# Kernel tuning notes

Hardware: AMD Instinct MI355X
Metric: run time of the kernel (lower is better)

The kernel has to match this reference:

```python
import jax, jax.numpy as jnp
import numpy as np

OPS = jnp.array([[1,1,1],[1,1,-1],[1,-1,1],[1,-1,-1],[-1,1,1],[-1,1,-1],[-1,-1,1],[-1,-1,-1]], dtype=jnp.float32)  # [8,3] sign flips per eigenvector column

B, N, FN, FE, E = 1, 512, 8, 1, 32
D0 = 6 + FN  # layer-0 node embedding dim: framed (x,v) = 6 dims + node features


def setup_inputs() -> dict:
    key = jax.random.key(0)
    ks = jax.random.split(key, 24)
    rn = lambda k, shp, s=0.1: jax.random.normal(k, shp, jnp.float32) * s
    inp = {
        'node_feat': jax.random.normal(ks[0], (B, N, FN), jnp.float32),
        'edge_feat': jax.random.normal(ks[1], (B, N, N, FE), jnp.float32),
        'x': jax.random.normal(ks[2], (B, N, 3), jnp.float32),
        'v': jax.random.normal(ks[3], (B, N, 3), jnp.float32),
        # GNN layer 0 (input node dim D0)
        'e0_w1': rn(ks[4], (FE + 2 * D0, E)), 'e0_b1': jnp.zeros((E,), jnp.float32),
        'e0_w2': rn(ks[5], (E, E)), 'e0_b2': jnp.zeros((E,), jnp.float32),
        'n0_w1': rn(ks[6], (D0 + E, E)), 'n0_b1': jnp.zeros((E,), jnp.float32),
        'n0_w2': rn(ks[7], (E, E)), 'n0_b2': jnp.zeros((E,), jnp.float32),
        # GNN layer 1 (input node dim E)
        'e1_w1': rn(ks[8], (FE + 2 * E, E)), 'e1_b1': jnp.zeros((E,), jnp.float32),
        'e1_w2': rn(ks[9], (E, E)), 'e1_b2': jnp.zeros((E,), jnp.float32),
        'n1_w1': rn(ks[10], (E + E, E)), 'n1_b1': jnp.zeros((E,), jnp.float32),
        'n1_w2': rn(ks[11], (E, E)), 'n1_b2': jnp.zeros((E,), jnp.float32),
        # decoder: relu -> Linear(E,E) -> relu -> Linear(E,6)
        'dec_w1': rn(ks[12], (E, E)), 'dec_b1': jnp.zeros((E,), jnp.float32),
        'dec_w2': rn(ks[13], (E, 6)), 'dec_b2': jnp.zeros((6,), jnp.float32),
        # v_coef: relu -> Linear(E,E) -> relu -> Linear(E,1)
        'vc_w1': rn(ks[14], (E, E)), 'vc_b1': jnp.zeros((E,), jnp.float32),
        'vc_w2': rn(ks[15], (E, 1)), 'vc_b2': jnp.zeros((1,), jnp.float32),
    }
    return inp


def _gnn_layer(h, edge_feat, ew1, eb1, ew2, eb2, nw1, nb1, nw2, nb2):
    # h: [B,N,d]; edge_feat: [B,N,N,Fe]
    # Torch builds concat([edge_feat, h_j, h_i]) per (i,j) pair; we split W1 rows
    # to avoid materializing the [B,N,N,Fe+2d] concat (same math).
    Fe = edge_feat.shape[-1]
    d = h.shape[-1]
    pre_e = edge_feat @ ew1[:Fe]          # [B,N,N,E]
    pre_j = h @ ew1[Fe:Fe + d]            # [B,N,E], indexed by j
    pre_i = h @ ew1[Fe + d:]              # [B,N,E], indexed by i
    m = jax.nn.relu(pre_e + pre_j[:, None, :, :] + pre_i[:, :, None, :] + eb1)
    m = jax.nn.relu(m @ ew2 + eb2)        # [B,N,N,E]
    agg = m.sum(axis=2)                   # sum over neighbors j -> [B,N,E]
    dn = jax.nn.relu(h @ nw1[:d] + agg @ nw1[d:] + nb1)
    return dn @ nw2 + nb2                 # [B,N,E]


def reference(node_feat, edge_feat, x, v,
              e0_w1, e0_b1, e0_w2, e0_b2, n0_w1, n0_b1, n0_w2, n0_b2,
              e1_w1, e1_b1, e1_w2, e1_b2, n1_w1, n1_b1, n1_w2, n1_b2,
              dec_w1, dec_b1, dec_w2, dec_b2, vc_w1, vc_b1, vc_w2, vc_b2):
    # ---- create_frame (PCA frame averaging) ----
    center = x.mean(axis=1, keepdims=True)                 # [B,1,3]
    xc = x - center
    R = jnp.einsum('bni,bnj->bij', xc, xc)                 # [B,3,3]
    _, Vv = jnp.linalg.eigh(R)                             # eigenvectors, ascending (like torch.symeig)
    F_ops = jax.lax.stop_gradient(OPS[None, :, None, :] * Vv[:, None, :, :])  # [B,8,3,3]
    center = jax.lax.stop_gradient(center)
    xc = x - center
    fx = jnp.einsum('boji,bnj->obni', F_ops, xc)           # [8,B,N,3] (F_ops^T applied)
    fv = jnp.einsum('boji,bnj->obni', F_ops, v)            # [8,B,N,3]
    nf = jnp.broadcast_to(node_feat[None], (8,) + node_feat.shape)
    h0 = jnp.concatenate([fx, fv, nf], axis=-1)            # [8,B,N,6+FN]

    l0 = (e0_w1, e0_b1, e0_w2, e0_b2, n0_w1, n0_b1, n0_w2, n0_b2)
    l1 = (e1_w1, e1_b1, e1_w2, e1_b2, n1_w1, n1_b1, n1_w2, n1_b2)
    frames = []
    for i in range(8):  # small fixed frame count; loop keeps N^2 intermediates per-frame
        hi = _gnn_layer(h0[i], edge_feat, *l0)
        hi = _gnn_layer(hi, edge_feat, *l1)
        frames.append(hi)
    h_out = jnp.stack(frames)                              # [8,B,N,E]

    # ---- decoder + invert_frame ----
    s = jax.nn.relu(jax.nn.relu(h_out) @ dec_w1 + dec_b1)
    spatial_out = s @ dec_w2 + dec_b2                      # [8,B,N,6]
    so = jnp.transpose(spatial_out, (1, 0, 2, 3))          # [B,8,N,6]
    dx = jnp.einsum('boij,bonj->bni', F_ops, so[..., :3]) / 8.0
    dv = jnp.einsum('boij,bonj->bni', F_ops, so[..., 3:]) / 8.0

    h_mean = h_out.mean(axis=0)                            # [B,N,E]
    coef = jax.nn.relu(jax.nn.relu(h_mean) @ vc_w1 + vc_b1) @ vc_w2 + vc_b2  # [B,N,1]
    v_out = v + dv
    x_out = x + v_out * coef + dx
    return (h_mean, edge_feat, x_out, v_out)
```

## Files before the change

### kernel.cpp

```cpp
#include <hip/hip_runtime.h>
#include <hip/hip_bf16.h>
#include <hip/hip_fp16.h>
#include <math.h>

#define NN 512

typedef _Float16 f16x8 __attribute__((ext_vector_type(8)));
typedef float    f32x4 __attribute__((ext_vector_type(4)));

__global__ void __launch_bounds__(256) frame_kernel(
    const float* __restrict__ x, float* __restrict__ FR,
    const float* __restrict__ e0w1, const float* __restrict__ e1w1,
    const float* __restrict__ e0w2, const float* __restrict__ e1w2,
    _Float16* __restrict__ WEH0, _Float16* __restrict__ WEH1,
    _Float16* __restrict__ W2F0, _Float16* __restrict__ W2F1) {
    __shared__ double red[4][9];
    int t = threadIdx.x;
    double s[9] = {0,0,0,0,0,0,0,0,0};
    for (int n = t; n < NN; n += 256) {
        double X = x[n*3+0], Y = x[n*3+1], Z = x[n*3+2];
        s[0]+=X; s[1]+=Y; s[2]+=Z;
        s[3]+=X*X; s[4]+=X*Y; s[5]+=X*Z; s[6]+=Y*Y; s[7]+=Y*Z; s[8]+=Z*Z;
    }
    #pragma unroll
    for (int m = 1; m < 64; m <<= 1) {
        #pragma unroll
        for (int q = 0; q < 9; ++q) s[q] += __shfl_xor(s[q], m);
    }
    int wave = t >> 6, lane = t & 63;
    if (lane == 0) {
        #pragma unroll
        for (int q = 0; q < 9; ++q) red[wave][q] = s[q];
    }
    __syncthreads();
    if (wave == 1) {
        int l15 = lane & 15, kb = (lane >> 4) * 8;
        #pragma unroll
        for (int e = 0; e < 8; ++e) {
            W2F0[lane*16 + e]     = (_Float16)e0w2[(kb+e)*32 + l15];
            W2F0[lane*16 + 8 + e] = (_Float16)e0w2[(kb+e)*32 + l15 + 16];
            W2F1[lane*16 + e]     = (_Float16)e1w2[(kb+e)*32 + l15];
            W2F1[lane*16 + 8 + e] = (_Float16)e1w2[(kb+e)*32 + l15 + 16];
        }
        if (lane < 32) { WEH0[lane] = (_Float16)e0w1[lane]; WEH1[lane] = (_Float16)e1w1[lane]; }
    }
    if (t == 0) {
        double S[9];
        #pragma unroll
        for (int q = 0; q < 9; ++q) S[q] = red[0][q]+red[1][q]+red[2][q]+red[3][q];
        double cx = S[0]/512.0, cy = S[1]/512.0, cz = S[2]/512.0;
        double A[3][3];
        A[0][0]=S[3]-512.0*cx*cx; A[0][1]=S[4]-512.0*cx*cy; A[0][2]=S[5]-512.0*cx*cz;
        A[1][1]=S[6]-512.0*cy*cy; A[1][2]=S[7]-512.0*cy*cz; A[2][2]=S[8]-512.0*cz*cz;
        A[1][0]=A[0][1]; A[2][0]=A[0][2]; A[2][1]=A[1][2];
        double V[3][3] = {{1,0,0},{0,1,0},{0,0,1}};
        for (int sweep = 0; sweep < 8; ++sweep) {
            double off = fabs(A[0][1]) + fabs(A[0][2]) + fabs(A[1][2]);
            double dia = fabs(A[0][0]) + fabs(A[1][1]) + fabs(A[2][2]);
            if (off < 1e-14 * (dia + 1e-300)) break;
            for (int p = 0; p < 3; ++p) for (int q = p+1; q < 3; ++q) {
                double apq = A[p][q];
                if (fabs(apq) < 1e-300) continue;
                double tau = (A[q][q] - A[p][p]) / (2.0 * apq);
                double tt = (tau >= 0 ? 1.0 : -1.0) / (fabs(tau) + sqrt(1.0 + tau*tau));
                double cc = 1.0 / sqrt(1.0 + tt*tt), ss = tt * cc;
                double apq2 = apq;
                A[p][p] = A[p][p] - tt * apq2;
                A[q][q] = A[q][q] + tt * apq2;
                A[p][q] = 0.0; A[q][p] = 0.0;
                for (int k = 0; k < 3; ++k) if (k != p && k != q) {
                    double akp = A[k][p], akq = A[k][q];
                    A[k][p] = cc*akp - ss*akq; A[p][k] = A[k][p];
                    A[k][q] = ss*akp + cc*akq; A[q][k] = A[k][q];
                }
                for (int k = 0; k < 3; ++k) {
                    double vkp = V[k][p], vkq = V[k][q];
                    V[k][p] = cc*vkp - ss*vkq;
                    V[k][q] = ss*vkp + cc*vkq;
                }
            }
        }
        double ev[3] = {A[0][0], A[1][1], A[2][2]};
        int idx[3] = {0,1,2};
        for (int a = 0; a < 2; ++a) for (int b = a+1; b < 3; ++b)
            if (ev[idx[b]] < ev[idx[a]]) { int tmp = idx[a]; idx[a] = idx[b]; idx[b] = tmp; }
        FR[0] = (float)cx; FR[1] = (float)cy; FR[2] = (float)cz;
        for (int r = 0; r < 3; ++r)
            for (int c = 0; c < 3; ++c)
                FR[3 + r*3 + c] = (float)V[r][idx[c]];
    }
}

__global__ void __launch_bounds__(256) pre0_kernel(const float* __restrict__ x,
                                                   const float* __restrict__ v,
                                                   const float* __restrict__ nf,
                                                   const float* __restrict__ FR,
                                                   const float* __restrict__ ew1,
                                                   const float* __restrict__ eb1,
                                                   float* __restrict__ H0,
                                                   _Float16* __restrict__ PJ,
                                                   _Float16* __restrict__ PIB) {
    int t = blockIdx.x * 256 + threadIdx.x;
    int c = t & 31, row = t >> 5;
    int o = row >> 9, j = row & 511;
    float hrow[14];
    float xc0 = x[j*3+0] - FR[0], xc1 = x[j*3+1] - FR[1], xc2 = x[j*3+2] - FR[2];
    float v0 = v[j*3+0], v1 = v[j*3+1], v2 = v[j*3+2];
    #pragma unroll
    for (int i = 0; i < 3; ++i) {
        float sgn = ((o >> (2 - i)) & 1) ? -1.f : 1.f;
        float px = FR[3 + 0*3 + i]*xc0 + FR[3 + 1*3 + i]*xc1 + FR[3 + 2*3 + i]*xc2;
        float pv = FR[3 + 0*3 + i]*v0  + FR[3 + 1*3 + i]*v1  + FR[3 + 2*3 + i]*v2;
        hrow[i]     = sgn * px;
        hrow[3 + i] = sgn * pv;
    }
    #pragma unroll
    for (int k = 0; k < 8; ++k) hrow[6 + k] = nf[j*8 + k];
    if (c < 14) H0[row * 14 + c] = hrow[c];
    float pj = 0.f, pi = eb1[c];
    #pragma unroll
    for (int k = 0; k < 14; ++k) {
        pj = fmaf(hrow[k], ew1[(1 + k) * 32 + c], pj);
        pi = fmaf(hrow[k], ew1[(15 + k) * 32 + c], pi);
    }
    PJ[row * 32 + c] = (_Float16)pj;
    PIB[row * 32 + c] = (_Float16)pi;
}

template<int D, bool NEXT>
__global__ void __launch_bounds__(256, 6) edge_kernel(
    const _Float16* __restrict__ PJH,
    const _Float16* __restrict__ PIH,
    const _Float16* __restrict__ WEH,
    const _Float16* __restrict__ W2F,
    const float* __restrict__ edge,
    const float* __restrict__ h,
    const float* __restrict__ eb2,
    const float* __restrict__ nw1,
    const float* __restrict__ nb1,
    const float* __restrict__ nw2,
    const float* __restrict__ nb2,
    float* __restrict__ hout,
    const float* __restrict__ ew1n,
    const float* __restrict__ eb1n,
    _Float16* __restrict__ PJn,
    _Float16* __restrict__ PIn)
{
    const int t = threadIdx.x;
    const int wv = t >> 6, lane = t & 63;
    const int o = blockIdx.x >> 8;
    const int i0 = (blockIdx.x & 255) << 1;
    const int i = i0 + (wv & 1);
    const int jh = wv >> 1;
    const int row = (o << 9) | i;
    const int l15 = lane & 15;
    const int kbase = (lane >> 4) * 8;

    __shared__ float sAgg[4][32];

    const f16x8 pi8 = *(const f16x8*)(PIH + row * 32 + kbase);
    const f16x8 we8 = *(const f16x8*)(WEH + kbase);
    const f16x8 bfrag0 = *(const f16x8*)(W2F + lane * 16);
    const f16x8 bfrag1 = *(const f16x8*)(W2F + lane * 16 + 8);
    const float b2v0 = eb2[l15], b2v1 = eb2[l15 + 16];
    const f16x8 z8 = {0,0,0,0,0,0,0,0};
    float agg0 = 0.f, agg1 = 0.f;

    const float* edge_i = edge + (i << 9);
    const _Float16* pj_o = PJH + ((size_t)(o << 9)) * 32;

    #pragma unroll
    for (int jt = 0; jt < 4; ++jt) {
        const int jtbase = ((jh << 2) | jt) << 6;
        #pragma unroll
        for (int jm = 0; jm < 4; ++jm) {
            const int j = jtbase + (jm << 4) + l15;
            const _Float16 eh = (_Float16)edge_i[j];
            const f16x8 e8 = {eh, eh, eh, eh, eh, eh, eh, eh};
            const f16x8 pj8 = *(const f16x8*)(pj_o + j * 32 + kbase);
            f16x8 m = e8 * we8 + (pj8 + pi8);
            m = __builtin_elementwise_max(m, z8);
            f32x4 c0 = {0.f, 0.f, 0.f, 0.f};
            c0 = __builtin_amdgcn_mfma_f32_16x16x32_f16(m, bfrag0, c0, 0, 0, 0);
            #pragma unroll
            for (int r = 0; r < 4; ++r) agg0 += fmaxf(c0[r] + b2v0, 0.f);
            f32x4 c1 = {0.f, 0.f, 0.f, 0.f};
            c1 = __builtin_amdgcn_mfma_f32_16x16x32_f16(m, bfrag1, c1, 0, 0, 0);
            #pragma unroll
            for (int r = 0; r < 4; ++r) agg1 += fmaxf(c1[r] + b2v1, 0.f);
        }
    }
    agg0 += __shfl_xor(agg0, 16); agg0 += __shfl_xor(agg0, 32);
    agg1 += __shfl_xor(agg1, 16); agg1 += __shfl_xor(agg1, 32);
    if (lane < 16) { sAgg[wv][l15] = agg0; sAgg[wv][16 + l15] = agg1; }
    __syncthreads();
    if (wv >= 2) return;

    const int c2 = lane & 31;
    const float red = sAgg[wv][c2] + sAgg[wv + 2][c2];
    const float* hr = h + row * D;
    float acc = nb1[c2];
    #pragma unroll
    for (int k = 0; k < D; ++k) acc = fmaf(hr[k], nw1[k * 32 + c2], acc);
    #pragma unroll
    for (int k = 0; k < 32; ++k)
        acc = fmaf(__shfl(red, k, 32), nw1[(D + k) * 32 + c2], acc);
    const float dn = fmaxf(acc, 0.f);
    float outv = nb2[c2];
    #pragma unroll
    for (int k = 0; k < 32; ++k)
        outv = fmaf(__shfl(dn, k, 32), nw2[k * 32 + c2], outv);
    if (lane < 32) hout[row * 32 + c2] = outv;

    if (NEXT) {
        float pj1 = 0.f, pi1 = eb1n[c2];
        #pragma unroll
        for (int k = 0; k < 32; ++k) {
            const float hk = __shfl(outv, k, 32);
            pj1 = fmaf(hk, ew1n[(1 + k) * 32 + c2], pj1);
            pi1 = fmaf(hk, ew1n[(33 + k) * 32 + c2], pi1);
        }
        if (lane < 32) {
            PJn[row * 32 + c2] = (_Float16)pj1;
            PIn[row * 32 + c2] = (_Float16)pi1;
        }
    }
}

__global__ void __launch_bounds__(256) decfinal_kernel(
    const float* __restrict__ h2,
    const float* __restrict__ w1, const float* __restrict__ b1,
    const float* __restrict__ w2,
    const float* __restrict__ b2,
    const float* __restrict__ x, const float* __restrict__ v,
    const float* __restrict__ FR,
    const float* __restrict__ vw1, const float* __restrict__ vb1,
    const float* __restrict__ vw2, const float* __restrict__ vb2,
    float* __restrict__ out_hmean, float* __restrict__ out_x,
    float* __restrict__ out_v)
{
    const int n = blockIdx.x;
    const int t = threadIdx.x;
    const int wv = t >> 6, lane = t & 63;
    const int c = lane & 31;
    __shared__ float sSo[8][6];

    #pragma unroll
    for (int q = 0; q < 2; ++q) {
        const int o = (wv << 1) | q;
        const int row = (o << 9) | n;
        float rh = fmaxf(h2[row * 32 + c], 0.f);
        float acc = b1[c];
        #pragma unroll
        for (int k = 0; k < 32; ++k)
            acc = fmaf(__shfl(rh, k, 32), w1[k * 32 + c], acc);
        float s = fmaxf(acc, 0.f);
        #pragma unroll
        for (int m = 0; m < 6; ++m) {
            float p = s * w2[c * 6 + m];
            p += __shfl_xor(p, 1); p += __shfl_xor(p, 2); p += __shfl_xor(p, 4);
            p += __shfl_xor(p, 8); p += __shfl_xor(p, 16);
            if (lane == 0) sSo[o][m] = p + b2[m];
        }
    }
    __syncthreads();
    if (wv) return;

    float hm = 0.f;
    #pragma unroll
    for (int o = 0; o < 8; ++o) hm += h2[((o << 9) | n) * 32 + c];
    hm *= 0.125f;
    if (lane < 32) out_hmean[n * 32 + c] = hm;
    float rh = fmaxf(hm, 0.f);
    float acc = vb1[c];
    #pragma unroll
    for (int k = 0; k < 32; ++k)
        acc = fmaf(__shfl(rh, k, 32), vw1[k * 32 + c], acc);
    float t1 = fmaxf(acc, 0.f);
    float p = t1 * vw2[c];
    p += __shfl_xor(p, 1); p += __shfl_xor(p, 2); p += __shfl_xor(p, 4);
    p += __shfl_xor(p, 8); p += __shfl_xor(p, 16);
    float coef = p + vb2[0];
    if (lane < 3) {
        int i = lane;
        float dx = 0.f, dv = 0.f;
        #pragma unroll
        for (int o = 0; o < 8; ++o) {
            #pragma unroll
            for (int j = 0; j < 3; ++j) {
                float sgn = ((o >> (2 - j)) & 1) ? -1.f : 1.f;
                float f = sgn * FR[3 + i * 3 + j];
                dx = fmaf(f, sSo[o][j], dx);
                dv = fmaf(f, sSo[o][3 + j], dv);
            }
        }
        dx *= 0.125f; dv *= 0.125f;
        float vout = v[n * 3 + i] + dv;
        out_v[n * 3 + i] = vout;
        out_x[n * 3 + i] = x[n * 3 + i] + vout * coef + dx;
    }
}

extern "C" void kernel_launch(void* const* d_in, const int* in_sizes, int n_in,
                              void* d_out, int out_size, void* d_ws, size_t ws_size,
                              hipStream_t stream) {
    const float* node_feat = (const float*)d_in[0];
    const float* edge      = (const float*)d_in[1];
    const float* x         = (const float*)d_in[2];
    const float* v         = (const float*)d_in[3];
    const float* e0_w1 = (const float*)d_in[4];
    const float* e0_b1 = (const float*)d_in[5];
    const float* e0_w2 = (const float*)d_in[6];
    const float* e0_b2 = (const float*)d_in[7];
    const float* n0_w1 = (const float*)d_in[8];
    const float* n0_b1 = (const float*)d_in[9];
    const float* n0_w2 = (const float*)d_in[10];
    const float* n0_b2 = (const float*)d_in[11];
    const float* e1_w1 = (const float*)d_in[12];
    const float* e1_b1 = (const float*)d_in[13];
    const float* e1_w2 = (const float*)d_in[14];
    const float* e1_b2 = (const float*)d_in[15];
    const float* n1_w1 = (const float*)d_in[16];
    const float* n1_b1 = (const float*)d_in[17];
    const float* n1_w2 = (const float*)d_in[18];
    const float* n1_b2 = (const float*)d_in[19];
    const float* dec_w1 = (const float*)d_in[20];
    const float* dec_b1 = (const float*)d_in[21];
    const float* dec_w2 = (const float*)d_in[22];
    const float* dec_b2 = (const float*)d_in[23];
    const float* vc_w1 = (const float*)d_in[24];
    const float* vc_b1 = (const float*)d_in[25];
    const float* vc_w2 = (const float*)d_in[26];
    const float* vc_b2 = (const float*)d_in[27];

    char* wsb = (char*)d_ws;
    float* out = (float*)d_out;

    float*    FR   = (float*)wsb;
    float*    H0   = (float*)(wsb + 256);
    float*    HA   = (float*)(wsb + 256 + 229376);
    float*    HB   = (float*)(wsb + 256 + 229376 + 524288);
    char*     p    = wsb + 256 + 229376 + 524288 + 524288;
    _Float16* PJH0 = (_Float16*)p;            p += 262144;
    _Float16* PIH0 = (_Float16*)p;            p += 262144;
    _Float16* PJH1 = (_Float16*)p;            p += 262144;
    _Float16* PIH1 = (_Float16*)p;            p += 262144;
    _Float16* WEH0 = (_Float16*)p;            p += 256;
    _Float16* WEH1 = (_Float16*)p;            p += 256;
    _Float16* W2F0 = (_Float16*)p;            p += 2048;
    _Float16* W2F1 = (_Float16*)p;            p += 2048;

    hipMemcpyAsync(out + 16384, edge, (size_t)262144 * sizeof(float),
                   hipMemcpyDeviceToDevice, stream);

    frame_kernel<<<1, 256, 0, stream>>>(x, FR, e0_w1, e1_w1, e0_w2, e1_w2,
                                        WEH0, WEH1, W2F0, W2F1);

    pre0_kernel<<<512, 256, 0, stream>>>(x, v, node_feat, FR, e0_w1, e0_b1,
                                         H0, PJH0, PIH0);
    edge_kernel<14, true><<<2048, 256, 0, stream>>>(
        PJH0, PIH0, WEH0, W2F0, edge, H0, e0_b2, n0_w1, n0_b1, n0_w2, n0_b2,
        HA, e1_w1, e1_b1, PJH1, PIH1);
    edge_kernel<32, false><<<2048, 256, 0, stream>>>(
        PJH1, PIH1, WEH1, W2F1, edge, HA, e1_b2, n1_w1, n1_b1, n1_w2, n1_b2,
        HB, nullptr, nullptr, nullptr, nullptr);
    decfinal_kernel<<<512, 256, 0, stream>>>(HB, dec_w1, dec_b1, dec_w2, dec_b2,
                                             x, v, FR, vc_w1, vc_b1, vc_w2, vc_b2,
                                             out, out + 278528, out + 280064);
}
```

Before: 163.4 us.

## Fuse frame computation and edge copy into pre0, pre-swizzle PJ into MFMA fragment layout

Removes the single-block frame kernel and the device-to-device memcpy. Each pre0 block now recomputes the PCA frame redundantly in shared memory and copies its slice of edge features to the output. Block 0 writes the shared weight conversions. PJ is stored in a fragment-contiguous layout so each lane of the edge kernel does one contiguous 16-byte load per tile, and the edge kernel's launch-bounds occupancy hint drops from 6 to 4. The cost is redundant per-block reductions over x and the Jacobi solve in every pre0 block.

```diff
diff --git a/kernel.cpp b/kernel.cpp
--- a/kernel.cpp
+++ b/kernel.cpp
@@ -8,14 +8,10 @@
 typedef _Float16 f16x8 __attribute__((ext_vector_type(8)));
 typedef float    f32x4 __attribute__((ext_vector_type(4)));
 
-__global__ void __launch_bounds__(256) frame_kernel(
-    const float* __restrict__ x, float* __restrict__ FR,
-    const float* __restrict__ e0w1, const float* __restrict__ e1w1,
-    const float* __restrict__ e0w2, const float* __restrict__ e1w2,
-    _Float16* __restrict__ WEH0, _Float16* __restrict__ WEH1,
-    _Float16* __restrict__ W2F0, _Float16* __restrict__ W2F1) {
-    __shared__ double red[4][9];
-    int t = threadIdx.x;
+__device__ __forceinline__ void compute_frame(const float* __restrict__ x,
+                                              float* __restrict__ sFR,
+                                              double (*red)[9]) {
+    const int t = threadIdx.x;
     double s[9] = {0,0,0,0,0,0,0,0,0};
     for (int n = t; n < NN; n += 256) {
         double X = x[n*3+0], Y = x[n*3+1], Z = x[n*3+2];
@@ -27,23 +23,12 @@
         #pragma unroll
         for (int q = 0; q < 9; ++q) s[q] += __shfl_xor(s[q], m);
     }
-    int wave = t >> 6, lane = t & 63;
+    const int wave = t >> 6, lane = t & 63;
     if (lane == 0) {
         #pragma unroll
         for (int q = 0; q < 9; ++q) red[wave][q] = s[q];
     }
     __syncthreads();
-    if (wave == 1) {
-        int l15 = lane & 15, kb = (lane >> 4) * 8;
-        #pragma unroll
-        for (int e = 0; e < 8; ++e) {
-            W2F0[lane*16 + e]     = (_Float16)e0w2[(kb+e)*32 + l15];
-            W2F0[lane*16 + 8 + e] = (_Float16)e0w2[(kb+e)*32 + l15 + 16];
-            W2F1[lane*16 + e]     = (_Float16)e1w2[(kb+e)*32 + l15];
-            W2F1[lane*16 + 8 + e] = (_Float16)e1w2[(kb+e)*32 + l15 + 16];
-        }
-        if (lane < 32) { WEH0[lane] = (_Float16)e0w1[lane]; WEH1[lane] = (_Float16)e1w1[lane]; }
-    }
     if (t == 0) {
         double S[9];
         #pragma unroll
@@ -64,9 +49,8 @@
                 double tau = (A[q][q] - A[p][p]) / (2.0 * apq);
                 double tt = (tau >= 0 ? 1.0 : -1.0) / (fabs(tau) + sqrt(1.0 + tau*tau));
                 double cc = 1.0 / sqrt(1.0 + tt*tt), ss = tt * cc;
-                double apq2 = apq;
-                A[p][p] = A[p][p] - tt * apq2;
-                A[q][q] = A[q][q] + tt * apq2;
+                A[p][p] = A[p][p] - tt * apq;
+                A[q][q] = A[q][q] + tt * apq;
                 A[p][q] = 0.0; A[q][p] = 0.0;
                 for (int k = 0; k < 3; ++k) if (k != p && k != q) {
                     double akp = A[k][p], akq = A[k][q];
@@ -84,52 +68,89 @@
         int idx[3] = {0,1,2};
         for (int a = 0; a < 2; ++a) for (int b = a+1; b < 3; ++b)
             if (ev[idx[b]] < ev[idx[a]]) { int tmp = idx[a]; idx[a] = idx[b]; idx[b] = tmp; }
-        FR[0] = (float)cx; FR[1] = (float)cy; FR[2] = (float)cz;
+        sFR[0] = (float)cx; sFR[1] = (float)cy; sFR[2] = (float)cz;
         for (int r = 0; r < 3; ++r)
             for (int c = 0; c < 3; ++c)
-                FR[3 + r*3 + c] = (float)V[r][idx[c]];
-    }
-}
-
-__global__ void __launch_bounds__(256) pre0_kernel(const float* __restrict__ x,
-                                                   const float* __restrict__ v,
-                                                   const float* __restrict__ nf,
-                                                   const float* __restrict__ FR,
-                                                   const float* __restrict__ ew1,
-                                                   const float* __restrict__ eb1,
-                                                   float* __restrict__ H0,
-                                                   _Float16* __restrict__ PJ,
-                                                   _Float16* __restrict__ PIB) {
-    int t = blockIdx.x * 256 + threadIdx.x;
-    int c = t & 31, row = t >> 5;
-    int o = row >> 9, j = row & 511;
+                sFR[3 + r*3 + c] = (float)V[r][idx[c]];
+    }
+    __syncthreads();
+}
+
+__global__ void __launch_bounds__(256) pre0_kernel(
+    const float* __restrict__ x, const float* __restrict__ v,
+    const float* __restrict__ nf,
+    const float* __restrict__ e0w1, const float* __restrict__ e0b1,
+    const float* __restrict__ e0w2, const float* __restrict__ e1w1,
+    const float* __restrict__ e1w2,
+    const float* __restrict__ edge,
+    float* __restrict__ FRg, float* __restrict__ H0,
+    _Float16* __restrict__ PJF, _Float16* __restrict__ PIH,
+    _Float16* __restrict__ WEH0, _Float16* __restrict__ WEH1,
+    _Float16* __restrict__ W2F0, _Float16* __restrict__ W2F1,
+    float* __restrict__ out_edge)
+{
+    __shared__ double red[4][9];
+    __shared__ float sFR[12];
+    const int t = threadIdx.x;
+    const int b = blockIdx.x;
+
+    compute_frame(x, sFR, red);
+
+    ((float2*)out_edge)[b * 256 + t] = ((const float2*)edge)[b * 256 + t];
+
+    if (b == 0) {
+        const int lane = t & 63, wv = t >> 6;
+        if (t < 12) FRg[t] = sFR[t];
+        const int l15 = lane & 15, kb = (lane >> 4) * 8;
+        if (wv == 1) {
+            #pragma unroll
+            for (int e = 0; e < 8; ++e) {
+                W2F0[lane*16 + e]     = (_Float16)e0w2[(kb+e)*32 + l15];
+                W2F0[lane*16 + 8 + e] = (_Float16)e0w2[(kb+e)*32 + l15 + 16];
+            }
+        } else if (wv == 2) {
+            #pragma unroll
+            for (int e = 0; e < 8; ++e) {
+                W2F1[lane*16 + e]     = (_Float16)e1w2[(kb+e)*32 + l15];
+                W2F1[lane*16 + 8 + e] = (_Float16)e1w2[(kb+e)*32 + l15 + 16];
+            }
+        } else if (wv == 3 && lane < 32) {
+            WEH0[lane] = (_Float16)e0w1[lane];
+            WEH1[lane] = (_Float16)e1w1[lane];
+        }
+    }
+
+    const int c = t & 31;
+    const int row = b * 8 + (t >> 5);
+    const int o = row >> 9, j = row & 511;
     float hrow[14];
-    float xc0 = x[j*3+0] - FR[0], xc1 = x[j*3+1] - FR[1], xc2 = x[j*3+2] - FR[2];
+    float xc0 = x[j*3+0] - sFR[0], xc1 = x[j*3+1] - sFR[1], xc2 = x[j*3+2] - sFR[2];
     float v0 = v[j*3+0], v1 = v[j*3+1], v2 = v[j*3+2];
     #pragma unroll
     for (int i = 0; i < 3; ++i) {
         float sgn = ((o >> (2 - i)) & 1) ? -1.f : 1.f;
-        float px = FR[3 + 0*3 + i]*xc0 + FR[3 + 1*3 + i]*xc1 + FR[3 + 2*3 + i]*xc2;
-        float pv = FR[3 + 0*3 + i]*v0  + FR[3 + 1*3 + i]*v1  + FR[3 + 2*3 + i]*v2;
+        float px = sFR[3 + 0*3 + i]*xc0 + sFR[3 + 1*3 + i]*xc1 + sFR[3 + 2*3 + i]*xc2;
+        float pv = sFR[3 + 0*3 + i]*v0  + sFR[3 + 1*3 + i]*v1  + sFR[3 + 2*3 + i]*v2;
         hrow[i]     = sgn * px;
         hrow[3 + i] = sgn * pv;
     }
     #pragma unroll
     for (int k = 0; k < 8; ++k) hrow[6 + k] = nf[j*8 + k];
     if (c < 14) H0[row * 14 + c] = hrow[c];
-    float pj = 0.f, pi = eb1[c];
+    float pj = 0.f, pi = e0b1[c];
     #pragma unroll
     for (int k = 0; k < 14; ++k) {
-        pj = fmaf(hrow[k], ew1[(1 + k) * 32 + c], pj);
-        pi = fmaf(hrow[k], ew1[(15 + k) * 32 + c], pi);
-    }
-    PJ[row * 32 + c] = (_Float16)pj;
-    PIB[row * 32 + c] = (_Float16)pi;
+        pj = fmaf(hrow[k], e0w1[(1 + k) * 32 + c], pj);
+        pi = fmaf(hrow[k], e0w1[(15 + k) * 32 + c], pi);
+    }
+    PIH[row * 32 + c] = (_Float16)pi;
+    const int fl = (j & 15) | ((c >> 3) << 4);
+    PJF[(((o << 5) + (j >> 4)) * 64 + fl) * 8 + (c & 7)] = (_Float16)pj;
 }
 
 template<int D, bool NEXT>
-__global__ void __launch_bounds__(256, 6) edge_kernel(
-    const _Float16* __restrict__ PJH,
+__global__ void __launch_bounds__(256, 4) edge_kernel(
+    const _Float16* __restrict__ PJF,
     const _Float16* __restrict__ PIH,
     const _Float16* __restrict__ WEH,
     const _Float16* __restrict__ W2F,
@@ -143,7 +164,7 @@
     float* __restrict__ hout,
     const float* __restrict__ ew1n,
     const float* __restrict__ eb1n,
-    _Float16* __restrict__ PJn,
+    _Float16* __restrict__ PJFn,
     _Float16* __restrict__ PIn)
 {
     const int t = threadIdx.x;
@@ -167,28 +188,24 @@
     float agg0 = 0.f, agg1 = 0.f;
 
     const float* edge_i = edge + (i << 9);
-    const _Float16* pj_o = PJH + ((size_t)(o << 9)) * 32;
-
-    #pragma unroll
-    for (int jt = 0; jt < 4; ++jt) {
-        const int jtbase = ((jh << 2) | jt) << 6;
-        #pragma unroll
-        for (int jm = 0; jm < 4; ++jm) {
-            const int j = jtbase + (jm << 4) + l15;
-            const _Float16 eh = (_Float16)edge_i[j];
-            const f16x8 e8 = {eh, eh, eh, eh, eh, eh, eh, eh};
-            const f16x8 pj8 = *(const f16x8*)(pj_o + j * 32 + kbase);
-            f16x8 m = e8 * we8 + (pj8 + pi8);
-            m = __builtin_elementwise_max(m, z8);
-            f32x4 c0 = {0.f, 0.f, 0.f, 0.f};
-            c0 = __builtin_amdgcn_mfma_f32_16x16x32_f16(m, bfrag0, c0, 0, 0, 0);
-            #pragma unroll
-            for (int r = 0; r < 4; ++r) agg0 += fmaxf(c0[r] + b2v0, 0.f);
-            f32x4 c1 = {0.f, 0.f, 0.f, 0.f};
-            c1 = __builtin_amdgcn_mfma_f32_16x16x32_f16(m, bfrag1, c1, 0, 0, 0);
-            #pragma unroll
-            for (int r = 0; r < 4; ++r) agg1 += fmaxf(c1[r] + b2v1, 0.f);
-        }
+    const _Float16* pjf_o = PJF + (size_t)o * 16384;
+
+    #pragma unroll
+    for (int jm = 0; jm < 16; ++jm) {
+        const int tile = (jh << 4) | jm;
+        const f16x8 pj8 = *(const f16x8*)(pjf_o + (tile * 64 + lane) * 8);
+        const _Float16 eh = (_Float16)edge_i[tile * 16 + l15];
+        const f16x8 e8 = {eh, eh, eh, eh, eh, eh, eh, eh};
+        f16x8 m = e8 * we8 + (pj8 + pi8);
+        m = __builtin_elementwise_max(m, z8);
+        f32x4 c0 = {0.f, 0.f, 0.f, 0.f};
+        c0 = __builtin_amdgcn_mfma_f32_16x16x32_f16(m, bfrag0, c0, 0, 0, 0);
+        #pragma unroll
+        for (int r = 0; r < 4; ++r) agg0 += fmaxf(c0[r] + b2v0, 0.f);
+        f32x4 c1 = {0.f, 0.f, 0.f, 0.f};
+        c1 = __builtin_amdgcn_mfma_f32_16x16x32_f16(m, bfrag1, c1, 0, 0, 0);
+        #pragma unroll
+        for (int r = 0; r < 4; ++r) agg1 += fmaxf(c1[r] + b2v1, 0.f);
     }
     agg0 += __shfl_xor(agg0, 16); agg0 += __shfl_xor(agg0, 32);
     agg1 += __shfl_xor(agg1, 16); agg1 += __shfl_xor(agg1, 32);
@@ -197,14 +214,14 @@
     if (wv >= 2) return;
 
     const int c2 = lane & 31;
-    const float red = sAgg[wv][c2] + sAgg[wv + 2][c2];
+    const float red2 = sAgg[wv][c2] + sAgg[wv + 2][c2];
     const float* hr = h + row * D;
     float acc = nb1[c2];
     #pragma unroll
     for (int k = 0; k < D; ++k) acc = fmaf(hr[k], nw1[k * 32 + c2], acc);
     #pragma unroll
     for (int k = 0; k < 32; ++k)
-        acc = fmaf(__shfl(red, k, 32), nw1[(D + k) * 32 + c2], acc);
+        acc = fmaf(__shfl(red2, k, 32), nw1[(D + k) * 32 + c2], acc);
     const float dn = fmaxf(acc, 0.f);
     float outv = nb2[c2];
     #pragma unroll
@@ -221,8 +238,9 @@
             pi1 = fmaf(hk, ew1n[(33 + k) * 32 + c2], pi1);
         }
         if (lane < 32) {
-            PJn[row * 32 + c2] = (_Float16)pj1;
             PIn[row * 32 + c2] = (_Float16)pi1;
+            const int fl = (i & 15) | ((c2 >> 3) << 4);
+            PJFn[(((o << 5) + (i >> 4)) * 64 + fl) * 8 + (c2 & 7)] = (_Float16)pj1;
         }
     }
 }
@@ -341,28 +359,24 @@
     float*    HA   = (float*)(wsb + 256 + 229376);
     float*    HB   = (float*)(wsb + 256 + 229376 + 524288);
     char*     p    = wsb + 256 + 229376 + 524288 + 524288;
-    _Float16* PJH0 = (_Float16*)p;            p += 262144;
+    _Float16* PJF0 = (_Float16*)p;            p += 262144;
     _Float16* PIH0 = (_Float16*)p;            p += 262144;
-    _Float16* PJH1 = (_Float16*)p;            p += 262144;
+    _Float16* PJF1 = (_Float16*)p;            p += 262144;
     _Float16* PIH1 = (_Float16*)p;            p += 262144;
     _Float16* WEH0 = (_Float16*)p;            p += 256;
     _Float16* WEH1 = (_Float16*)p;            p += 256;
     _Float16* W2F0 = (_Float16*)p;            p += 2048;
     _Float16* W2F1 = (_Float16*)p;            p += 2048;
 
-    hipMemcpyAsync(out + 16384, edge, (size_t)262144 * sizeof(float),
-                   hipMemcpyDeviceToDevice, stream);
-
-    frame_kernel<<<1, 256, 0, stream>>>(x, FR, e0_w1, e1_w1, e0_w2, e1_w2,
-                                        WEH0, WEH1, W2F0, W2F1);
-
-    pre0_kernel<<<512, 256, 0, stream>>>(x, v, node_feat, FR, e0_w1, e0_b1,
-                                         H0, PJH0, PIH0);
+    pre0_kernel<<<512, 256, 0, stream>>>(x, v, node_feat,
+                                         e0_w1, e0_b1, e0_w2, e1_w1, e1_w2,
+                                         edge, FR, H0, PJF0, PIH0,
+                                         WEH0, WEH1, W2F0, W2F1, out + 16384);
     edge_kernel<14, true><<<2048, 256, 0, stream>>>(
-        PJH0, PIH0, WEH0, W2F0, edge, H0, e0_b2, n0_w1, n0_b1, n0_w2, n0_b2,
-        HA, e1_w1, e1_b1, PJH1, PIH1);
+        PJF0, PIH0, WEH0, W2F0, edge, H0, e0_b2, n0_w1, n0_b1, n0_w2, n0_b2,
+        HA, e1_w1, e1_b1, PJF1, PIH1);
     edge_kernel<32, false><<<2048, 256, 0, stream>>>(
-        PJH1, PIH1, WEH1, W2F1, edge, HA, e1_b2, n1_w1, n1_b1, n1_w2, n1_b2,
+        PJF1, PIH1, WEH1, W2F1, edge, HA, e1_b2, n1_w1, n1_b1, n1_w2, n1_b2,
         HB, nullptr, nullptr, nullptr, nullptr);
     decfinal_kernel<<<512, 256, 0, stream>>>(HB, dec_w1, dec_b1, dec_w2, dec_b2,
                                              x, v, FR, vc_w1, vc_b1, vc_w2, vc_b2,
```

New measurement: 154.8 us. 1.06x faster.
